# Kernel optimization log

Hardware: AMD Instinct MI355X
Metric: run time of the kernel (lower is better)

## Reference

```python
import jax, jax.numpy as jnp
import numpy as np
import math

WINDOW_SIZE = 11
SIGMA = 1.5


def _gaussian_window(window_size=WINDOW_SIZE, sigma=SIGMA):
    # Faithful port of get_gaussian_kernel (separable gaussian, normalized to sum 1)
    c = (window_size - 1) / 2
    ax = (np.arange(window_size) - c) ** 2
    dist = ax[:, None, None] + ax[None, :, None] + ax[None, None, :]
    denom = math.sqrt(2 * math.pi) * sigma
    w = np.exp(-dist / (2 * sigma ** 2)) / denom ** 2
    w = w / w.sum()
    return jnp.asarray(w[None, None], dtype=jnp.float32)  # [1,1,k,k,k] (OIDHW)


def setup_inputs() -> dict:
    key = jax.random.key(0)
    k1, k2 = jax.random.split(key)
    D = H = W = 192
    gr = jax.random.normal(k1, (1, D, H, W), dtype=jnp.float32)
    gt = jax.random.normal(k2, (1, D, H, W), dtype=jnp.float32)
    window = _gaussian_window()
    return {"gr": gr, "gt": gt, "window": window}


def _local_conv(x, window):
    # x: [N,1,D,H,W]; 'SAME' padding == padding=window_size//2 for odd kernel
    return jax.lax.conv_general_dilated(
        x, window, window_strides=(1, 1, 1), padding='SAME',
        dimension_numbers=('NCDHW', 'OIDHW', 'NCDHW'))


def reference(gr, gt, window):
    # get_ssim_loss: rescale from [-1,1] to [0,1], add batch dim -> [1,1,D,H,W]
    gr = ((gr + 1) / 2)[None]
    gt = ((gt + 1) / 2)[None]

    mu1 = _local_conv(gr, window)
    mu2 = _local_conv(gt, window)
    mu1_sq = mu1 * mu1
    mu2_sq = mu2 * mu2
    mu1_mu2 = mu1 * mu2
    sigma1_sq = _local_conv(gr * gr, window) - mu1_sq
    sigma2_sq = _local_conv(gt * gt, window) - mu2_sq
    sigma12 = _local_conv(gr * gt, window) - mu1_mu2

    C1 = 0.01 ** 2
    C2 = 0.03 ** 2
    ssim_map = ((2 * mu1_mu2 + C1) * (2 * sigma12 + C2)) / (
        (mu1_sq + mu2_sq + C1) * (sigma1_sq + sigma2_sq + C2))
    ssim = jnp.mean(ssim_map)
    return 1.0 - ssim
```

## Files before the change

### kernel.cpp

```cpp
#include <hip/hip_runtime.h>
#include <hip/hip_fp16.h>
#include <math.h>
#include <string.h>

#define Dd 192
#define Hh 192
#define Ww 192
#define K  11
#define R  5

#define DC 16
#define NP 26

typedef _Float16 h4  __attribute__((ext_vector_type(4)));
typedef float    f32x4 __attribute__((ext_vector_type(4)));

struct GWF { float gf[K]; unsigned int g2[K]; };

static __device__ __forceinline__ __half2 u2h2(unsigned int u) {
    union { unsigned int u; __half2 h; } x; x.u = u; return x.h;
}
static __device__ __forceinline__ unsigned int h22u(__half2 h) {
    union { __half2 h; unsigned int u; } x; x.h = h; return x.u;
}
static __device__ __forceinline__ unsigned int pk(float a, float b) {
    typedef __fp16 f16x2 __attribute__((ext_vector_type(2)));
    f16x2 r = __builtin_amdgcn_cvt_pkrtz(a, b);
    union { f16x2 v; unsigned int u; } x; x.v = r; return x.u;
}
static __device__ __forceinline__ float wsel(int j, const GWF& G) {
    float v = 0.f;
#pragma unroll
    for (int t = 0; t < K; ++t) v = (j == t) ? G.gf[t] : v;
    return v;
}
static __device__ __forceinline__ f32x4 MFMA(unsigned int a0, unsigned int a1,
                                             unsigned int b0, unsigned int b1,
                                             f32x4 c) {
    union { unsigned int u[2]; h4 h; } A, B;
    A.u[0] = a0; A.u[1] = a1; B.u[0] = b0; B.u[1] = b1;
    return __builtin_amdgcn_mfma_f32_16x16x16f16(A.h, B.h, c, 0, 0, 0);
}

__global__ __launch_bounds__(256, 2) void fused_ssim(
    const float* __restrict__ gr, const float* __restrict__ gt,
    GWF gw, double* __restrict__ acc_g)
{
    __shared__ float wsum[4];

    const int tid  = threadIdx.x;
    const int wv   = tid >> 6;
    const int lane = tid & 63;
    const int n16  = lane & 15;
    const int g4   = lane >> 4;

    const int bid  = blockIdx.x;
    const int wgid = (bid & 7) * 54 + (bid >> 3);
    const int z4   = wgid % 12;
    const int yx   = wgid / 12;
    const int hy   = yx % 12;
    const int bx   = yx / 12;

    const int w0 = (bx * 4 + wv) * 16;
    const int h0 = hy * 16;
    const int d0 = z4 * DC;

    int addr[2][2]; float amf[2][2];
#pragma unroll
    for (int rc = 0; rc < 2; ++rc)
#pragma unroll
    for (int kc = 0; kc < 2; ++kc) {
        const int gh   = h0 - R + 16 * rc + n16;
        const bool rok = (gh >= 0) && (gh < Hh);
        const int ghc  = gh < 0 ? 0 : (gh >= Hh ? Hh - 1 : gh);
        const int gx   = w0 - 8 + 16 * kc + 4 * g4;
        const bool cok = (gx >= 0) && (gx + 3 < Ww);
        const int gxc  = gx < 0 ? 0 : (gx > Ww - 4 ? Ww - 4 : gx);
        addr[rc][kc] = ghc * Ww + gxc;
        amf[rc][kc]  = (rok && cok) ? 0.5f : 0.f;
    }

    unsigned int Bw[2][2];
#pragma unroll
    for (int kc = 0; kc < 2; ++kc) {
        const int kb = 16 * kc + 4 * g4 - n16 - 3;
        Bw[kc][0] = pk(wsel(kb + 0, gw), wsel(kb + 1, gw));
        Bw[kc][1] = pk(wsel(kb + 2, gw), wsel(kb + 3, gw));
    }
    unsigned int Ah[2][2];
#pragma unroll
    for (int kc = 0; kc < 2; ++kc) {
        const int kb = 16 * kc + 4 * g4 - n16;
        Ah[kc][0] = pk(wsel(kb + 0, gw), wsel(kb + 1, gw));
        Ah[kc][1] = pk(wsel(kb + 2, gw), wsel(kb + 3, gw));
    }

    float4 px[2][2], py[2][2];
    auto LOADP = [&](int p) {
        const int z  = d0 - R + p;
        const bool zok = (z >= 0) && (z < Dd);
        const int zb = (zok ? z : 0) * Hh * Ww;
#pragma unroll
        for (int rc = 0; rc < 2; ++rc)
#pragma unroll
        for (int kc = 0; kc < 2; ++kc) {
            px[rc][kc] = *(const float4*)(gr + zb + addr[rc][kc]);
            py[rc][kc] = *(const float4*)(gt + zb + addr[rc][kc]);
        }
    };

    unsigned int hist[K][5][2];
#pragma unroll
    for (int t = 0; t < K; ++t)
#pragma unroll
        for (int f = 0; f < 5; ++f) { hist[t][f][0] = 0u; hist[t][f][1] = 0u; }

    float ssim_acc = 0.0f;
    LOADP(0);

    for (int c = 0; c < 3; ++c) {
#pragma unroll
        for (int j = 0; j < K; ++j) {
            const int ip = c * K + j;
            if (ip < NP) {
                const int z = d0 - R + ip;
                const bool zok = (z >= 0) && (z < Dd);

                unsigned int b2[5][2][2];
#pragma unroll
                for (int rc = 0; rc < 2; ++rc) {
                    unsigned int stgf[5][2][2];
#pragma unroll
                    for (int kc = 0; kc < 2; ++kc) {
                        const float A = zok ? amf[rc][kc] : 0.f;
                        const float4 X = px[rc][kc], Y = py[rc][kc];
                        const float xs0 = fmaf(X.x, A, A), xs1 = fmaf(X.y, A, A);
                        const float xs2 = fmaf(X.z, A, A), xs3 = fmaf(X.w, A, A);
                        const float ys0 = fmaf(Y.x, A, A), ys1 = fmaf(Y.y, A, A);
                        const float ys2 = fmaf(Y.z, A, A), ys3 = fmaf(Y.w, A, A);
                        stgf[0][kc][0] = pk(xs0, xs1);          stgf[0][kc][1] = pk(xs2, xs3);
                        stgf[1][kc][0] = pk(ys0, ys1);          stgf[1][kc][1] = pk(ys2, ys3);
                        stgf[2][kc][0] = pk(xs0*xs0, xs1*xs1);  stgf[2][kc][1] = pk(xs2*xs2, xs3*xs3);
                        stgf[3][kc][0] = pk(ys0*ys0, ys1*ys1);  stgf[3][kc][1] = pk(ys2*ys2, ys3*ys3);
                        stgf[4][kc][0] = pk(xs0*ys0, xs1*ys1);  stgf[4][kc][1] = pk(xs2*ys2, xs3*ys3);
                    }
#pragma unroll
                    for (int f = 0; f < 5; ++f) {
                        f32x4 cw = {0.f, 0.f, 0.f, 0.f};
                        cw = MFMA(stgf[f][0][0], stgf[f][0][1], Bw[0][0], Bw[0][1], cw);
                        cw = MFMA(stgf[f][1][0], stgf[f][1][1], Bw[1][0], Bw[1][1], cw);
                        b2[f][rc][0] = pk(cw[0], cw[1]);
                        b2[f][rc][1] = pk(cw[2], cw[3]);
                    }
                }

                if (ip + 1 < NP) LOADP(ip + 1);

#pragma unroll
                for (int f = 0; f < 5; ++f) {
                    f32x4 ch = {0.f, 0.f, 0.f, 0.f};
                    ch = MFMA(Ah[0][0], Ah[0][1], b2[f][0][0], b2[f][0][1], ch);
                    ch = MFMA(Ah[1][0], Ah[1][1], b2[f][1][0], b2[f][1][1], ch);
                    hist[j][f][0] = pk(ch[0], ch[1]);
                    hist[j][f][1] = pk(ch[2], ch[3]);
                }

                if (ip >= 2 * R) {
                    __half2 s[5][2];
#pragma unroll
                    for (int f = 0; f < 5; ++f) { s[f][0] = u2h2(0u); s[f][1] = u2h2(0u); }
#pragma unroll
                    for (int t7 = 0; t7 < K; ++t7) {
                        const int sl = (j + 1 + t7) % K;
                        const __half2 g = u2h2(gw.g2[t7]);
#pragma unroll
                        for (int f = 0; f < 5; ++f) {
                            s[f][0] = __hfma2(g, u2h2(hist[sl][f][0]), s[f][0]);
                            s[f][1] = __hfma2(g, u2h2(hist[sl][f][1]), s[f][1]);
                        }
                    }
                    const float C1 = 1e-4f, C2 = 9e-4f;
#pragma unroll
                    for (int p = 0; p < 2; ++p) {
#pragma unroll
                        for (int col = 0; col < 2; ++col) {
                            const float m1  = col ? __high2float(s[0][p]) : __low2float(s[0][p]);
                            const float m2  = col ? __high2float(s[1][p]) : __low2float(s[1][p]);
                            const float e11 = col ? __high2float(s[2][p]) : __low2float(s[2][p]);
                            const float e22 = col ? __high2float(s[3][p]) : __low2float(s[3][p]);
                            const float e12 = col ? __high2float(s[4][p]) : __low2float(s[4][p]);
                            const float mu1sq = m1 * m1, mu2sq = m2 * m2, mu12 = m1 * m2;
                            const float s11 = e11 - mu1sq;
                            const float s22 = e22 - mu2sq;
                            const float s12 = e12 - mu12;
                            const float num = (2.f * mu12 + C1) * (2.f * s12 + C2);
                            const float den = (mu1sq + mu2sq + C1) * (s11 + s22 + C2);
                            ssim_acc += num * __builtin_amdgcn_rcpf(den);
                        }
                    }
                }
            }
        }
    }

    float v = ssim_acc;
#pragma unroll
    for (int o = 32; o > 0; o >>= 1) v += __shfl_down(v, o);
    if (lane == 0) wsum[wv] = v;
    __syncthreads();
    if (tid == 0) atomicAdd(acc_g, (double)(wsum[0] + wsum[1] + wsum[2] + wsum[3]));
}

__global__ void k4_final(const double* __restrict__ acc, float* __restrict__ out) {
    if (threadIdx.x == 0) {
        const double n = (double)((size_t)Dd * Hh * Ww);
        out[0] = (float)(1.0 - (*acc) / n);
    }
}

static unsigned short f2h(float x) {
    unsigned int u; memcpy(&u, &x, 4);
    unsigned int s = (u >> 16) & 0x8000u;
    int e = (int)((u >> 23) & 0xffu) - 112;
    unsigned int m = u & 0x7fffffu;
    if (e <= 0) return (unsigned short)s;
    unsigned int mant = m + 0xFFFu + ((m >> 13) & 1u);
    if (mant & 0x800000u) { mant = 0; e += 1; }
    return (unsigned short)(s | ((unsigned)e << 10) | (mant >> 13));
}

extern "C" void kernel_launch(void* const* d_in, const int* in_sizes, int n_in,
                              void* d_out, int out_size, void* d_ws, size_t ws_size,
                              hipStream_t stream) {
    const float* gr = (const float*)d_in[0];
    const float* gt = (const float*)d_in[1];
    float* out = (float*)d_out;

    GWF gw;
    {
        double e[K], s = 0.0;
        for (int i = 0; i < K; ++i) {
            const double a = (double)((i - R) * (i - R));
            e[i] = exp(-a / (2.0 * 1.5 * 1.5));
            s += e[i];
        }
        for (int i = 0; i < K; ++i) {
            gw.gf[i] = (float)(e[i] / s);
            unsigned short h = f2h(gw.gf[i]);
            gw.g2[i] = (unsigned int)h | ((unsigned int)h << 16);
        }
    }

    double* acc = (double*)d_ws;
    (void)hipMemsetAsync(d_ws, 0, sizeof(double), stream);

    fused_ssim<<<432, 256, 0, stream>>>(gr, gt, gw, acc);

    k4_final<<<1, 64, 0, stream>>>(acc, out);
}
```

Baseline: 64.25 us.

## Use single-wave blocks with shorter depth chunks and half-precision products

Work is split into single-wavefront blocks (2304 blocks of 64 threads), and each block covers a depth chunk of 12 instead of 16. This raises parallelism and drops the shared-memory reduction and barrier, since every wave now does its own double atomic. The squared and cross products are computed as packed fp16 multiplies on already-converted halves instead of in fp32, and the prefetch is issued before the horizontal MFMA stage. In exchange there is more halo recomputation per output (22 planes for 12 outputs), more atomics, and some precision loss from the fp16 products.

```diff
diff --git a/kernel.cpp b/kernel.cpp
--- a/kernel.cpp
+++ b/kernel.cpp
@@ -9,8 +9,8 @@
 #define K  11
 #define R  5
 
-#define DC 16
-#define NP 26
+#define DC 12
+#define NP 22
 
 typedef _Float16 h4  __attribute__((ext_vector_type(4)));
 typedef float    f32x4 __attribute__((ext_vector_type(4)));
@@ -27,6 +27,9 @@
     typedef __fp16 f16x2 __attribute__((ext_vector_type(2)));
     f16x2 r = __builtin_amdgcn_cvt_pkrtz(a, b);
     union { f16x2 v; unsigned int u; } x; x.v = r; return x.u;
+}
+static __device__ __forceinline__ unsigned int hmul2u(unsigned int a, unsigned int b) {
+    return h22u(__hmul2(u2h2(a), u2h2(b)));
 }
 static __device__ __forceinline__ float wsel(int j, const GWF& G) {
     float v = 0.f;
@@ -42,26 +45,22 @@
     return __builtin_amdgcn_mfma_f32_16x16x16f16(A.h, B.h, c, 0, 0, 0);
 }
 
-__global__ __launch_bounds__(256, 2) void fused_ssim(
+__global__ __launch_bounds__(64, 2) void fused_ssim(
     const float* __restrict__ gr, const float* __restrict__ gt,
     GWF gw, double* __restrict__ acc_g)
 {
-    __shared__ float wsum[4];
-
-    const int tid  = threadIdx.x;
-    const int wv   = tid >> 6;
-    const int lane = tid & 63;
+    const int lane = threadIdx.x & 63;
     const int n16  = lane & 15;
     const int g4   = lane >> 4;
 
     const int bid  = blockIdx.x;
-    const int wgid = (bid & 7) * 54 + (bid >> 3);
-    const int z4   = wgid % 12;
-    const int yx   = wgid / 12;
+    const int wgid = (bid & 7) * 288 + (bid >> 3);
+    const int z4   = wgid % 16;
+    const int yx   = wgid / 16;
     const int hy   = yx % 12;
     const int bx   = yx / 12;
 
-    const int w0 = (bx * 4 + wv) * 16;
+    const int w0 = bx * 16;
     const int h0 = hy * 16;
     const int d0 = z4 * DC;
 
@@ -118,85 +117,85 @@
     float ssim_acc = 0.0f;
     LOADP(0);
 
-    for (int c = 0; c < 3; ++c) {
+    for (int c = 0; c < 2; ++c) {
 #pragma unroll
         for (int j = 0; j < K; ++j) {
             const int ip = c * K + j;
-            if (ip < NP) {
-                const int z = d0 - R + ip;
-                const bool zok = (z >= 0) && (z < Dd);
-
-                unsigned int b2[5][2][2];
-#pragma unroll
-                for (int rc = 0; rc < 2; ++rc) {
-                    unsigned int stgf[5][2][2];
-#pragma unroll
-                    for (int kc = 0; kc < 2; ++kc) {
-                        const float A = zok ? amf[rc][kc] : 0.f;
-                        const float4 X = px[rc][kc], Y = py[rc][kc];
-                        const float xs0 = fmaf(X.x, A, A), xs1 = fmaf(X.y, A, A);
-                        const float xs2 = fmaf(X.z, A, A), xs3 = fmaf(X.w, A, A);
-                        const float ys0 = fmaf(Y.x, A, A), ys1 = fmaf(Y.y, A, A);
-                        const float ys2 = fmaf(Y.z, A, A), ys3 = fmaf(Y.w, A, A);
-                        stgf[0][kc][0] = pk(xs0, xs1);          stgf[0][kc][1] = pk(xs2, xs3);
-                        stgf[1][kc][0] = pk(ys0, ys1);          stgf[1][kc][1] = pk(ys2, ys3);
-                        stgf[2][kc][0] = pk(xs0*xs0, xs1*xs1);  stgf[2][kc][1] = pk(xs2*xs2, xs3*xs3);
-                        stgf[3][kc][0] = pk(ys0*ys0, ys1*ys1);  stgf[3][kc][1] = pk(ys2*ys2, ys3*ys3);
-                        stgf[4][kc][0] = pk(xs0*ys0, xs1*ys1);  stgf[4][kc][1] = pk(xs2*ys2, xs3*ys3);
-                    }
+            const int z = d0 - R + ip;
+            const bool zok = (z >= 0) && (z < Dd);
+
+            unsigned int stgf[2][5][2][2];
+#pragma unroll
+            for (int rc = 0; rc < 2; ++rc)
+#pragma unroll
+            for (int kc = 0; kc < 2; ++kc) {
+                const float A = zok ? amf[rc][kc] : 0.f;
+                const float4 X = px[rc][kc], Y = py[rc][kc];
+                const unsigned int hx0 = pk(fmaf(X.x, A, A), fmaf(X.y, A, A));
+                const unsigned int hx1 = pk(fmaf(X.z, A, A), fmaf(X.w, A, A));
+                const unsigned int hy0 = pk(fmaf(Y.x, A, A), fmaf(Y.y, A, A));
+                const unsigned int hy1 = pk(fmaf(Y.z, A, A), fmaf(Y.w, A, A));
+                stgf[rc][0][kc][0] = hx0;            stgf[rc][0][kc][1] = hx1;
+                stgf[rc][1][kc][0] = hy0;            stgf[rc][1][kc][1] = hy1;
+                stgf[rc][2][kc][0] = hmul2u(hx0,hx0); stgf[rc][2][kc][1] = hmul2u(hx1,hx1);
+                stgf[rc][3][kc][0] = hmul2u(hy0,hy0); stgf[rc][3][kc][1] = hmul2u(hy1,hy1);
+                stgf[rc][4][kc][0] = hmul2u(hx0,hy0); stgf[rc][4][kc][1] = hmul2u(hx1,hy1);
+            }
+
+            if (ip + 1 < NP) LOADP(ip + 1);
+
+            unsigned int b2[5][2][2];
+#pragma unroll
+            for (int rc = 0; rc < 2; ++rc)
+#pragma unroll
+            for (int f = 0; f < 5; ++f) {
+                f32x4 cw = {0.f, 0.f, 0.f, 0.f};
+                cw = MFMA(stgf[rc][f][0][0], stgf[rc][f][0][1], Bw[0][0], Bw[0][1], cw);
+                cw = MFMA(stgf[rc][f][1][0], stgf[rc][f][1][1], Bw[1][0], Bw[1][1], cw);
+                b2[f][rc][0] = pk(cw[0], cw[1]);
+                b2[f][rc][1] = pk(cw[2], cw[3]);
+            }
+
+#pragma unroll
+            for (int f = 0; f < 5; ++f) {
+                f32x4 ch = {0.f, 0.f, 0.f, 0.f};
+                ch = MFMA(Ah[0][0], Ah[0][1], b2[f][0][0], b2[f][0][1], ch);
+                ch = MFMA(Ah[1][0], Ah[1][1], b2[f][1][0], b2[f][1][1], ch);
+                hist[j][f][0] = pk(ch[0], ch[1]);
+                hist[j][f][1] = pk(ch[2], ch[3]);
+            }
+
+            if (ip >= 2 * R) {
+                __half2 s[5][2];
+#pragma unroll
+                for (int f = 0; f < 5; ++f) { s[f][0] = u2h2(0u); s[f][1] = u2h2(0u); }
+#pragma unroll
+                for (int t7 = 0; t7 < K; ++t7) {
+                    const int sl = (j + 1 + t7) % K;
+                    const __half2 g = u2h2(gw.g2[t7]);
 #pragma unroll
                     for (int f = 0; f < 5; ++f) {
-                        f32x4 cw = {0.f, 0.f, 0.f, 0.f};
-                        cw = MFMA(stgf[f][0][0], stgf[f][0][1], Bw[0][0], Bw[0][1], cw);
-                        cw = MFMA(stgf[f][1][0], stgf[f][1][1], Bw[1][0], Bw[1][1], cw);
-                        b2[f][rc][0] = pk(cw[0], cw[1]);
-                        b2[f][rc][1] = pk(cw[2], cw[3]);
+                        s[f][0] = __hfma2(g, u2h2(hist[sl][f][0]), s[f][0]);
+                        s[f][1] = __hfma2(g, u2h2(hist[sl][f][1]), s[f][1]);
                     }
                 }
-
-                if (ip + 1 < NP) LOADP(ip + 1);
-
-#pragma unroll
-                for (int f = 0; f < 5; ++f) {
-                    f32x4 ch = {0.f, 0.f, 0.f, 0.f};
-                    ch = MFMA(Ah[0][0], Ah[0][1], b2[f][0][0], b2[f][0][1], ch);
-                    ch = MFMA(Ah[1][0], Ah[1][1], b2[f][1][0], b2[f][1][1], ch);
-                    hist[j][f][0] = pk(ch[0], ch[1]);
-                    hist[j][f][1] = pk(ch[2], ch[3]);
-                }
-
-                if (ip >= 2 * R) {
-                    __half2 s[5][2];
-#pragma unroll
-                    for (int f = 0; f < 5; ++f) { s[f][0] = u2h2(0u); s[f][1] = u2h2(0u); }
-#pragma unroll
-                    for (int t7 = 0; t7 < K; ++t7) {
-                        const int sl = (j + 1 + t7) % K;
-                        const __half2 g = u2h2(gw.g2[t7]);
-#pragma unroll
-                        for (int f = 0; f < 5; ++f) {
-                            s[f][0] = __hfma2(g, u2h2(hist[sl][f][0]), s[f][0]);
-                            s[f][1] = __hfma2(g, u2h2(hist[sl][f][1]), s[f][1]);
-                        }
-                    }
-                    const float C1 = 1e-4f, C2 = 9e-4f;
-#pragma unroll
-                    for (int p = 0; p < 2; ++p) {
-#pragma unroll
-                        for (int col = 0; col < 2; ++col) {
-                            const float m1  = col ? __high2float(s[0][p]) : __low2float(s[0][p]);
-                            const float m2  = col ? __high2float(s[1][p]) : __low2float(s[1][p]);
-                            const float e11 = col ? __high2float(s[2][p]) : __low2float(s[2][p]);
-                            const float e22 = col ? __high2float(s[3][p]) : __low2float(s[3][p]);
-                            const float e12 = col ? __high2float(s[4][p]) : __low2float(s[4][p]);
-                            const float mu1sq = m1 * m1, mu2sq = m2 * m2, mu12 = m1 * m2;
-                            const float s11 = e11 - mu1sq;
-                            const float s22 = e22 - mu2sq;
-                            const float s12 = e12 - mu12;
-                            const float num = (2.f * mu12 + C1) * (2.f * s12 + C2);
-                            const float den = (mu1sq + mu2sq + C1) * (s11 + s22 + C2);
-                            ssim_acc += num * __builtin_amdgcn_rcpf(den);
-                        }
+                const float C1 = 1e-4f, C2 = 9e-4f;
+#pragma unroll
+                for (int p = 0; p < 2; ++p) {
+#pragma unroll
+                    for (int col = 0; col < 2; ++col) {
+                        const float m1  = col ? __high2float(s[0][p]) : __low2float(s[0][p]);
+                        const float m2  = col ? __high2float(s[1][p]) : __low2float(s[1][p]);
+                        const float e11 = col ? __high2float(s[2][p]) : __low2float(s[2][p]);
+                        const float e22 = col ? __high2float(s[3][p]) : __low2float(s[3][p]);
+                        const float e12 = col ? __high2float(s[4][p]) : __low2float(s[4][p]);
+                        const float mu1sq = m1 * m1, mu2sq = m2 * m2, mu12 = m1 * m2;
+                        const float s11 = e11 - mu1sq;
+                        const float s22 = e22 - mu2sq;
+                        const float s12 = e12 - mu12;
+                        const float num = (2.f * mu12 + C1) * (2.f * s12 + C2);
+                        const float den = (mu1sq + mu2sq + C1) * (s11 + s22 + C2);
+                        ssim_acc += num * __builtin_amdgcn_rcpf(den);
                     }
                 }
             }
@@ -206,9 +205,7 @@
     float v = ssim_acc;
 #pragma unroll
     for (int o = 32; o > 0; o >>= 1) v += __shfl_down(v, o);
-    if (lane == 0) wsum[wv] = v;
-    __syncthreads();
-    if (tid == 0) atomicAdd(acc_g, (double)(wsum[0] + wsum[1] + wsum[2] + wsum[3]));
+    if (lane == 0) atomicAdd(acc_g, (double)v);
 }
 
 __global__ void k4_final(const double* __restrict__ acc, float* __restrict__ out) {
@@ -254,7 +251,7 @@
     double* acc = (double*)d_ws;
     (void)hipMemsetAsync(d_ws, 0, sizeof(double), stream);
 
-    fused_ssim<<<432, 256, 0, stream>>>(gr, gt, gw, acc);
+    fused_ssim<<<2304, 64, 0, stream>>>(gr, gt, gw, acc);
 
     k4_final<<<1, 64, 0, stream>>>(acc, out);
 }
```

Result: slower. 93.16 us (+45.0%).

## Restructure separable MFMA conv: transposed input layout, reuse single weight operand, fp16 products

Applied to the files above, without the earlier changes.

Loads the input plane transposed (rows along the K dimension, columns along N) so both the W and H passes can use the same Bw weight B-operand, dropping the separate Ah weight fragments. Squares and cross products are now computed in packed fp16 after conversion instead of in fp32. The plane loop is fully unrolled over all 26 planes. Loads become scalar per-element gathers instead of float4, which raises the global load instruction count and may hurt coalescing, and fp16 products slightly lower precision.

```diff
diff --git a/kernel.cpp b/kernel.cpp
--- a/kernel.cpp
+++ b/kernel.cpp
@@ -27,6 +27,9 @@
     typedef __fp16 f16x2 __attribute__((ext_vector_type(2)));
     f16x2 r = __builtin_amdgcn_cvt_pkrtz(a, b);
     union { f16x2 v; unsigned int u; } x; x.v = r; return x.u;
+}
+static __device__ __forceinline__ unsigned int hmul2u(unsigned int a, unsigned int b) {
+    return h22u(__hmul2(u2h2(a), u2h2(b)));
 }
 static __device__ __forceinline__ float wsel(int j, const GWF& G) {
     float v = 0.f;
@@ -65,19 +68,22 @@
     const int h0 = hy * 16;
     const int d0 = z4 * DC;
 
-    int addr[2][2]; float amf[2][2];
-#pragma unroll
-    for (int rc = 0; rc < 2; ++rc)
-#pragma unroll
-    for (int kc = 0; kc < 2; ++kc) {
-        const int gh   = h0 - R + 16 * rc + n16;
-        const bool rok = (gh >= 0) && (gh < Hh);
-        const int ghc  = gh < 0 ? 0 : (gh >= Hh ? Hh - 1 : gh);
-        const int gx   = w0 - 8 + 16 * kc + 4 * g4;
-        const bool cok = (gx >= 0) && (gx + 3 < Ww);
-        const int gxc  = gx < 0 ? 0 : (gx > Ww - 4 ? Ww - 4 : gx);
-        addr[rc][kc] = ghc * Ww + gxc;
-        amf[rc][kc]  = (rok && cok) ? 0.5f : 0.f;
+    int addr[2][2][4]; float amf[2][2][4];
+#pragma unroll
+    for (int kc = 0; kc < 2; ++kc)
+#pragma unroll
+    for (int i = 0; i < 4; ++i) {
+        const int row  = h0 - 8 + 16 * kc + 4 * g4 + i;
+        const bool rok = (row >= 0) && (row < Hh);
+        const int rcl  = row < 0 ? 0 : (row >= Hh ? Hh - 1 : row);
+#pragma unroll
+        for (int c16 = 0; c16 < 2; ++c16) {
+            const int col  = w0 - 8 + 16 * c16 + n16;
+            const bool cok = (col >= 0) && (col < Ww);
+            const int ccl  = col < 0 ? 0 : (col >= Ww ? Ww - 1 : col);
+            addr[kc][c16][i] = rcl * Ww + ccl;
+            amf[kc][c16][i]  = (rok && cok) ? 0.5f : 0.f;
+        }
     }
 
     unsigned int Bw[2][2];
@@ -87,25 +93,20 @@
         Bw[kc][0] = pk(wsel(kb + 0, gw), wsel(kb + 1, gw));
         Bw[kc][1] = pk(wsel(kb + 2, gw), wsel(kb + 3, gw));
     }
-    unsigned int Ah[2][2];
-#pragma unroll
-    for (int kc = 0; kc < 2; ++kc) {
-        const int kb = 16 * kc + 4 * g4 - n16;
-        Ah[kc][0] = pk(wsel(kb + 0, gw), wsel(kb + 1, gw));
-        Ah[kc][1] = pk(wsel(kb + 2, gw), wsel(kb + 3, gw));
-    }
-
-    float4 px[2][2], py[2][2];
+
+    float pxv[2][2][4], pyv[2][2][4];
     auto LOADP = [&](int p) {
-        const int z  = d0 - R + p;
-        const bool zok = (z >= 0) && (z < Dd);
-        const int zb = (zok ? z : 0) * Hh * Ww;
-#pragma unroll
-        for (int rc = 0; rc < 2; ++rc)
-#pragma unroll
-        for (int kc = 0; kc < 2; ++kc) {
-            px[rc][kc] = *(const float4*)(gr + zb + addr[rc][kc]);
-            py[rc][kc] = *(const float4*)(gt + zb + addr[rc][kc]);
+        const int z_ = d0 - R + p;
+        const bool zok_ = (z_ >= 0) && (z_ < Dd);
+        const int zb_ = (zok_ ? z_ : 0) * Hh * Ww;
+#pragma unroll
+        for (int kc = 0; kc < 2; ++kc)
+#pragma unroll
+        for (int c16 = 0; c16 < 2; ++c16)
+#pragma unroll
+        for (int i = 0; i < 4; ++i) {
+            pxv[kc][c16][i] = gr[zb_ + addr[kc][c16][i]];
+            pyv[kc][c16][i] = gt[zb_ + addr[kc][c16][i]];
         }
     };
 
@@ -118,86 +119,90 @@
     float ssim_acc = 0.0f;
     LOADP(0);
 
-    for (int c = 0; c < 3; ++c) {
-#pragma unroll
-        for (int j = 0; j < K; ++j) {
-            const int ip = c * K + j;
-            if (ip < NP) {
-                const int z = d0 - R + ip;
-                const bool zok = (z >= 0) && (z < Dd);
-
-                unsigned int b2[5][2][2];
-#pragma unroll
-                for (int rc = 0; rc < 2; ++rc) {
-                    unsigned int stgf[5][2][2];
-#pragma unroll
-                    for (int kc = 0; kc < 2; ++kc) {
-                        const float A = zok ? amf[rc][kc] : 0.f;
-                        const float4 X = px[rc][kc], Y = py[rc][kc];
-                        const float xs0 = fmaf(X.x, A, A), xs1 = fmaf(X.y, A, A);
-                        const float xs2 = fmaf(X.z, A, A), xs3 = fmaf(X.w, A, A);
-                        const float ys0 = fmaf(Y.x, A, A), ys1 = fmaf(Y.y, A, A);
-                        const float ys2 = fmaf(Y.z, A, A), ys3 = fmaf(Y.w, A, A);
-                        stgf[0][kc][0] = pk(xs0, xs1);          stgf[0][kc][1] = pk(xs2, xs3);
-                        stgf[1][kc][0] = pk(ys0, ys1);          stgf[1][kc][1] = pk(ys2, ys3);
-                        stgf[2][kc][0] = pk(xs0*xs0, xs1*xs1);  stgf[2][kc][1] = pk(xs2*xs2, xs3*xs3);
-                        stgf[3][kc][0] = pk(ys0*ys0, ys1*ys1);  stgf[3][kc][1] = pk(ys2*ys2, ys3*ys3);
-                        stgf[4][kc][0] = pk(xs0*ys0, xs1*ys1);  stgf[4][kc][1] = pk(xs2*ys2, xs3*ys3);
-                    }
-#pragma unroll
-                    for (int f = 0; f < 5; ++f) {
-                        f32x4 cw = {0.f, 0.f, 0.f, 0.f};
-                        cw = MFMA(stgf[f][0][0], stgf[f][0][1], Bw[0][0], Bw[0][1], cw);
-                        cw = MFMA(stgf[f][1][0], stgf[f][1][1], Bw[1][0], Bw[1][1], cw);
-                        b2[f][rc][0] = pk(cw[0], cw[1]);
-                        b2[f][rc][1] = pk(cw[2], cw[3]);
-                    }
+#pragma unroll
+    for (int ip = 0; ip < NP; ++ip) {
+        const int j = ip % K;
+        const int z = d0 - R + ip;
+        const bool zok = (z >= 0) && (z < Dd);
+
+        unsigned int stgf[2][2][5][2];
+#pragma unroll
+        for (int kc = 0; kc < 2; ++kc)
+#pragma unroll
+        for (int c16 = 0; c16 < 2; ++c16) {
+            const float A0 = zok ? amf[kc][c16][0] : 0.f;
+            const float A1 = zok ? amf[kc][c16][1] : 0.f;
+            const float A2_ = zok ? amf[kc][c16][2] : 0.f;
+            const float A3 = zok ? amf[kc][c16][3] : 0.f;
+            const unsigned int hx0 = pk(fmaf(pxv[kc][c16][0], A0, A0),
+                                        fmaf(pxv[kc][c16][1], A1, A1));
+            const unsigned int hx1 = pk(fmaf(pxv[kc][c16][2], A2_, A2_),
+                                        fmaf(pxv[kc][c16][3], A3, A3));
+            const unsigned int hy0 = pk(fmaf(pyv[kc][c16][0], A0, A0),
+                                        fmaf(pyv[kc][c16][1], A1, A1));
+            const unsigned int hy1 = pk(fmaf(pyv[kc][c16][2], A2_, A2_),
+                                        fmaf(pyv[kc][c16][3], A3, A3));
+            stgf[kc][c16][0][0] = hx0;             stgf[kc][c16][0][1] = hx1;
+            stgf[kc][c16][1][0] = hy0;             stgf[kc][c16][1][1] = hy1;
+            stgf[kc][c16][2][0] = hmul2u(hx0,hx0); stgf[kc][c16][2][1] = hmul2u(hx1,hx1);
+            stgf[kc][c16][3][0] = hmul2u(hy0,hy0); stgf[kc][c16][3][1] = hmul2u(hy1,hy1);
+            stgf[kc][c16][4][0] = hmul2u(hx0,hy0); stgf[kc][c16][4][1] = hmul2u(hx1,hy1);
+        }
+
+        if (ip + 1 < NP) LOADP(ip + 1);
+
+        unsigned int a2[5][2][2];
+#pragma unroll
+        for (int c16 = 0; c16 < 2; ++c16)
+#pragma unroll
+        for (int f = 0; f < 5; ++f) {
+            f32x4 dh = {0.f, 0.f, 0.f, 0.f};
+            dh = MFMA(stgf[0][c16][f][0], stgf[0][c16][f][1], Bw[0][0], Bw[0][1], dh);
+            dh = MFMA(stgf[1][c16][f][0], stgf[1][c16][f][1], Bw[1][0], Bw[1][1], dh);
+            a2[f][c16][0] = pk(dh[0], dh[1]);
+            a2[f][c16][1] = pk(dh[2], dh[3]);
+        }
+
+#pragma unroll
+        for (int f = 0; f < 5; ++f) {
+            f32x4 o = {0.f, 0.f, 0.f, 0.f};
+            o = MFMA(a2[f][0][0], a2[f][0][1], Bw[0][0], Bw[0][1], o);
+            o = MFMA(a2[f][1][0], a2[f][1][1], Bw[1][0], Bw[1][1], o);
+            hist[j][f][0] = pk(o[0], o[1]);
+            hist[j][f][1] = pk(o[2], o[3]);
+        }
+
+        if (ip >= 2 * R) {
+            __half2 s[5][2];
+#pragma unroll
+            for (int f = 0; f < 5; ++f) { s[f][0] = u2h2(0u); s[f][1] = u2h2(0u); }
+#pragma unroll
+            for (int t7 = 0; t7 < K; ++t7) {
+                const int sl = (j + 1 + t7) % K;
+                const __half2 g = u2h2(gw.g2[t7]);
+#pragma unroll
+                for (int f = 0; f < 5; ++f) {
+                    s[f][0] = __hfma2(g, u2h2(hist[sl][f][0]), s[f][0]);
+                    s[f][1] = __hfma2(g, u2h2(hist[sl][f][1]), s[f][1]);
                 }
-
-                if (ip + 1 < NP) LOADP(ip + 1);
-
-#pragma unroll
-                for (int f = 0; f < 5; ++f) {
-                    f32x4 ch = {0.f, 0.f, 0.f, 0.f};
-                    ch = MFMA(Ah[0][0], Ah[0][1], b2[f][0][0], b2[f][0][1], ch);
-                    ch = MFMA(Ah[1][0], Ah[1][1], b2[f][1][0], b2[f][1][1], ch);
-                    hist[j][f][0] = pk(ch[0], ch[1]);
-                    hist[j][f][1] = pk(ch[2], ch[3]);
-                }
-
-                if (ip >= 2 * R) {
-                    __half2 s[5][2];
-#pragma unroll
-                    for (int f = 0; f < 5; ++f) { s[f][0] = u2h2(0u); s[f][1] = u2h2(0u); }
-#pragma unroll
-                    for (int t7 = 0; t7 < K; ++t7) {
-                        const int sl = (j + 1 + t7) % K;
-                        const __half2 g = u2h2(gw.g2[t7]);
-#pragma unroll
-                        for (int f = 0; f < 5; ++f) {
-                            s[f][0] = __hfma2(g, u2h2(hist[sl][f][0]), s[f][0]);
-                            s[f][1] = __hfma2(g, u2h2(hist[sl][f][1]), s[f][1]);
-                        }
-                    }
-                    const float C1 = 1e-4f, C2 = 9e-4f;
-#pragma unroll
-                    for (int p = 0; p < 2; ++p) {
-#pragma unroll
-                        for (int col = 0; col < 2; ++col) {
-                            const float m1  = col ? __high2float(s[0][p]) : __low2float(s[0][p]);
-                            const float m2  = col ? __high2float(s[1][p]) : __low2float(s[1][p]);
-                            const float e11 = col ? __high2float(s[2][p]) : __low2float(s[2][p]);
-                            const float e22 = col ? __high2float(s[3][p]) : __low2float(s[3][p]);
-                            const float e12 = col ? __high2float(s[4][p]) : __low2float(s[4][p]);
-                            const float mu1sq = m1 * m1, mu2sq = m2 * m2, mu12 = m1 * m2;
-                            const float s11 = e11 - mu1sq;
-                            const float s22 = e22 - mu2sq;
-                            const float s12 = e12 - mu12;
-                            const float num = (2.f * mu12 + C1) * (2.f * s12 + C2);
-                            const float den = (mu1sq + mu2sq + C1) * (s11 + s22 + C2);
-                            ssim_acc += num * __builtin_amdgcn_rcpf(den);
-                        }
-                    }
+            }
+            const float C1 = 1e-4f, C2 = 9e-4f;
+#pragma unroll
+            for (int p = 0; p < 2; ++p) {
+#pragma unroll
+                for (int col = 0; col < 2; ++col) {
+                    const float m1  = col ? __high2float(s[0][p]) : __low2float(s[0][p]);
+                    const float m2  = col ? __high2float(s[1][p]) : __low2float(s[1][p]);
+                    const float e11 = col ? __high2float(s[2][p]) : __low2float(s[2][p]);
+                    const float e22 = col ? __high2float(s[3][p]) : __low2float(s[3][p]);
+                    const float e12 = col ? __high2float(s[4][p]) : __low2float(s[4][p]);
+                    const float mu1sq = m1 * m1, mu2sq = m2 * m2, mu12 = m1 * m2;
+                    const float s11 = e11 - mu1sq;
+                    const float s22 = e22 - mu2sq;
+                    const float s12 = e12 - mu12;
+                    const float num = (2.f * mu12 + C1) * (2.f * s12 + C2);
+                    const float den = (mu1sq + mu2sq + C1) * (s11 + s22 + C2);
+                    ssim_acc += num * __builtin_amdgcn_rcpf(den);
                 }
             }
         }
```

Result: slower. 225.2 us (+250.5%).
